# Kernel optimization log

Measured on AMD Instinct MI355X. Metric: run time of the kernel, lower is better.

## Reference

```python
import jax, jax.numpy as jnp
import numpy as np

B, Hd, Wd, C, NH, WS = 8, 128, 128, 192, 6, 8
HDIM = int(C * 2.0)   # FFN hidden = 384
RED = C // 8          # AIM channel-gate reduction = 24


def setup_inputs() -> dict:
    key = jax.random.key(0)
    ks = jax.random.split(key, 12)
    s = 0.02
    return {
        "x": jax.random.normal(ks[0], (B, Hd * Wd, C), jnp.float32),
        "H": Hd,
        "W": Wd,
        "n1_w": jnp.ones((C,), jnp.float32),
        "n1_b": jnp.zeros((C,), jnp.float32),
        "qkv_w": jax.random.normal(ks[1], (C, 3 * C), jnp.float32) * s,
        "proj_w": jax.random.normal(ks[2], (C, C), jnp.float32) * s,
        "proj_b": jnp.zeros((C,), jnp.float32),
        "attn_bias": jax.random.normal(ks[3], (NH, WS * WS, WS * WS), jnp.float32) * s,
        "conv_w": jax.random.normal(ks[4], (C, 1, 3, 3), jnp.float32) * s,
        "cg_w1": jax.random.normal(ks[5], (RED, C), jnp.float32) * s,
        "cg_w2": jax.random.normal(ks[6], (C, RED), jnp.float32) * s,
        "n2_w": jnp.ones((C,), jnp.float32),
        "n2_b": jnp.zeros((C,), jnp.float32),
        "fc1_w": jax.random.normal(ks[7], (C, HDIM), jnp.float32) * s,
        "smix_w": jax.random.normal(ks[8], (HDIM, 1, 3, 3), jnp.float32) * s,
        "fc2_w": jax.random.normal(ks[9], (HDIM, C), jnp.float32) * s,
    }


def _ln(x, w, b):
    m = x.mean(-1, keepdims=True)
    v = ((x - m) ** 2).mean(-1, keepdims=True)
    return (x - m) * jax.lax.rsqrt(v + 1e-5) * w + b


def _dwconv(x, w, H, W):
    # x: [B, L, Cx] -> depthwise 3x3 'same' conv -> [B, L, Cx]
    Bx, L, Cx = x.shape
    xi = x.transpose(0, 2, 1).reshape(Bx, Cx, H, W)
    y = jax.lax.conv_general_dilated(
        xi, w, (1, 1), 'SAME', feature_group_count=Cx,
        dimension_numbers=('NCHW', 'OIHW', 'NCHW'))
    return y.reshape(Bx, Cx, L).transpose(0, 2, 1)


def _window_attn(x, H, W, qkv_w, proj_w, proj_b, bias):
    Bx, L, Cx = x.shape
    nHw, nWw = H // WS, W // WS  # H, W are multiples of WS here (no padding needed)
    hd = Cx // NH
    # [B, L, C] -> [B*nH*nW, ws*ws, C]
    xw = (x.reshape(Bx, nHw, WS, nWw, WS, Cx)
           .transpose(0, 1, 3, 2, 4, 5)
           .reshape(Bx * nHw * nWw, WS * WS, Cx))
    qkv = (xw @ qkv_w).reshape(-1, WS * WS, 3, NH, hd).transpose(2, 0, 3, 1, 4)
    q, k, v = qkv[0], qkv[1], qkv[2]          # [Bw, nh, N, hd]
    logits = (q * hd ** -0.5) @ k.transpose(0, 1, 3, 2) + bias[None]
    attn = jax.nn.softmax(logits, axis=-1)
    out = (attn @ v).transpose(0, 2, 1, 3).reshape(-1, WS * WS, Cx)
    out = out @ proj_w + proj_b
    # windows -> [B, L, C]
    return (out.reshape(Bx, nHw, nWw, WS, WS, Cx)
               .transpose(0, 1, 3, 2, 4, 5)
               .reshape(Bx, L, Cx))


def reference(x, H, W, n1_w, n1_b, qkv_w, proj_w, proj_b, attn_bias,
              conv_w, cg_w1, cg_w2, n2_w, n2_b, fc1_w, smix_w, fc2_w):
    n1 = _ln(x, n1_w, n1_b)
    attn_feat = _window_attn(n1, H, W, qkv_w, proj_w, proj_b, attn_bias)
    conv_feat = jax.nn.gelu(_dwconv(n1, conv_w, H, W), approximate=False)
    # AIM: channel_modulates_spatial (btype == 'spatial')
    pooled = conv_feat.mean(axis=1)                                   # [B, C]
    cm = jax.nn.sigmoid(jax.nn.gelu(pooled @ cg_w1.T, approximate=False) @ cg_w2.T)
    x = x + attn_feat * cm[:, None, :] + conv_feat                    # residual (DropPath=id)
    # FFN with depthwise spatial mixing
    n2 = _ln(x, n2_w, n2_b)
    h = jax.nn.gelu(n2 @ fc1_w, approximate=False)                    # [B, L, HDIM]
    h = _dwconv(h, smix_w, H, W)
    return x + h @ fc2_w
```

## Files before the change

### kernel.cpp

```cpp
#include <hip/hip_runtime.h>
#include <hip/hip_bf16.h>
#include <math.h>

#define BATCH 8
#define CCH 192
#define LTOK 16384
#define BL 131072LL
#define NWIN 2048
#define NHEADS 6

typedef __hip_bfloat16 bf16;
typedef __bf16 bfr;
typedef bfr bf16x8 __attribute__((ext_vector_type(8)));
typedef float f32x4 __attribute__((ext_vector_type(4)));
typedef unsigned short u16x8 __attribute__((ext_vector_type(8)));
typedef unsigned short u16x4 __attribute__((ext_vector_type(4)));
typedef unsigned int u32x2 __attribute__((ext_vector_type(2)));

#define FX     0
#define FN1W   1
#define FN1B   2
#define FQKVW  3
#define FPROJW 4
#define FPROJB 5
#define FBIAS  6
#define FCONVW 7
#define FCG1   8
#define FCG2   9
#define FN2W   10
#define FN2B   11
#define FFC1   12
#define FSMIX  13
#define FFC2   14

struct InPtrs { const void* p[15]; int n[15]; };

__device__ __forceinline__ float ldin(const void* p, long long i, int f32) {
    return f32 ? ((const float*)p)[i]
               : __bfloat162float(((const bf16*)p)[i]);
}

__device__ __forceinline__ float bfcvt(unsigned short u) {
    return __uint_as_float((unsigned)u << 16);
}

__device__ __forceinline__ f32x4 ld4f(const void* p, long long i, int f32) {
    if (f32) return *(const f32x4*)((const float*)p + i);
    u16x4 v = *(const u16x4*)((const bf16*)p + i);
    f32x4 r;
    r[0] = bfcvt(v[0]); r[1] = bfcvt(v[1]); r[2] = bfcvt(v[2]); r[3] = bfcvt(v[3]);
    return r;
}
__device__ __forceinline__ f32x4 ld4b(const bf16* p, long long i) {
    u16x4 v = *(const u16x4*)(p + i);
    f32x4 r;
    r[0] = bfcvt(v[0]); r[1] = bfcvt(v[1]); r[2] = bfcvt(v[2]); r[3] = bfcvt(v[3]);
    return r;
}
__device__ __forceinline__ void st4b(bf16* p, long long i, f32x4 v) {
    union { bf16 h; unsigned short u; } cv;
    u16x4 o;
    cv.h = __float2bfloat16(v[0]); o[0] = cv.u;
    cv.h = __float2bfloat16(v[1]); o[1] = cv.u;
    cv.h = __float2bfloat16(v[2]); o[2] = cv.u;
    cv.h = __float2bfloat16(v[3]); o[3] = cv.u;
    *(u16x4*)(p + i) = o;
}

__device__ __forceinline__ unsigned pk2bf(float a, float b) {
    union { bf16 h; unsigned short u; } ca, cb;
    ca.h = __float2bfloat16(a);
    cb.h = __float2bfloat16(b);
    return (unsigned)ca.u | ((unsigned)cb.u << 16);
}

__device__ __forceinline__ float gelu_f(float v) {
    return 0.5f * v * (1.0f + erff(v * 0.70710678118654752f));
}

__device__ int local_probe(const void* p_, int n) {
    __shared__ int sh0, sh1, sh2;
    if (threadIdx.x == 0) { sh0 = 0; sh1 = 0; sh2 = 0; }
    __syncthreads();
    const bf16* p = (const bf16*)p_;
    int m = n < 2048 ? n : 2048;
    bool insane = false, evennz = false, oddnz = false;
    for (int i = threadIdx.x; i < m; i += 256) {
        float v = __bfloat162float(p[i]);
        if (!(fabsf(v) <= 1e9f)) insane = true;
        if (v != 0.0f) { if (i & 1) oddnz = true; else evennz = true; }
    }
    if (insane) sh0 = 1;
    if (evennz) sh1 = 1;
    if (oddnz)  sh2 = 1;
    __syncthreads();
    return (sh0 || (!sh1 && sh2)) ? 1 : 0;
}

__global__ __launch_bounds__(256)
void prep_k(InPtrs ip, int* __restrict__ flags,
            bf16* __restrict__ qkv_wT, bf16* __restrict__ proj_wT,
            bf16* __restrict__ fc1_wT, bf16* __restrict__ fc2_wT,
            float* __restrict__ convwT, float* __restrict__ smixwT,
            float* __restrict__ pooled) {
    int blk = blockIdx.x;
    if (blk < 15) {
        int f = local_probe(ip.p[blk], ip.n[blk]);
        if (threadIdx.x == 0) flags[blk] = f;
        return;
    }
    blk -= 15;
    if (blk < 432) {
        int f = local_probe(ip.p[FQKVW], ip.n[FQKVW]);
        int idx = blk * 256 + threadIdx.x;
        int k = idx / 576, n = idx - k * 576;
        qkv_wT[(long long)n * 192 + k] = __float2bfloat16(ldin(ip.p[FQKVW], idx, f));
        return;
    }
    blk -= 432;
    if (blk < 144) {
        int f = local_probe(ip.p[FPROJW], ip.n[FPROJW]);
        int idx = blk * 256 + threadIdx.x;
        int k = idx / 192, n = idx - k * 192;
        proj_wT[(long long)n * 192 + k] = __float2bfloat16(ldin(ip.p[FPROJW], idx, f));
        return;
    }
    blk -= 144;
    if (blk < 288) {
        int f = local_probe(ip.p[FFC1], ip.n[FFC1]);
        int idx = blk * 256 + threadIdx.x;
        int k = idx / 384, n = idx - k * 384;
        fc1_wT[(long long)n * 192 + k] = __float2bfloat16(ldin(ip.p[FFC1], idx, f));
        return;
    }
    blk -= 288;
    if (blk < 288) {
        int f = local_probe(ip.p[FFC2], ip.n[FFC2]);
        int idx = blk * 256 + threadIdx.x;
        int k = idx / 192, n = idx - k * 192;
        fc2_wT[(long long)n * 384 + k] = __float2bfloat16(ldin(ip.p[FFC2], idx, f));
        return;
    }
    blk -= 288;
    if (blk < 7) {
        int f = local_probe(ip.p[FCONVW], ip.n[FCONVW]);
        int idx = blk * 256 + threadIdx.x;
        if (idx < 192 * 9) {
            int c = idx / 9, t = idx - c * 9;
            convwT[t * 192 + c] = ldin(ip.p[FCONVW], idx, f);
        }
        return;
    }
    blk -= 7;
    if (blk < 14) {
        int f = local_probe(ip.p[FSMIX], ip.n[FSMIX]);
        int idx = blk * 256 + threadIdx.x;
        if (idx < 384 * 9) {
            int c = idx / 9, t = idx - c * 9;
            smixwT[t * 384 + c] = ldin(ip.p[FSMIX], idx, f);
        }
        return;
    }
    blk -= 14;
    {
        int idx = blk * 256 + threadIdx.x;
        if (idx < BATCH * CCH) pooled[idx] = 0.f;
    }
}

__global__ __launch_bounds__(256)
void ln_kernel(const void* __restrict__ x, const void* __restrict__ w,
               const void* __restrict__ b, bf16* __restrict__ out,
               const int* flags) {
    int fx = flags[FX], fw = flags[FN1W], fb = flags[FN1B];
    int wv = threadIdx.x >> 6, lane = threadIdx.x & 63;
    int gw = lane >> 4, l16 = lane & 15;
    long long t = (long long)blockIdx.x * 16 + wv * 4 + gw;
    long long base = t * CCH;
    f32x4 v[3];
#pragma unroll
    for (int k = 0; k < 3; ++k)
        v[k] = ld4f(x, base + l16 * 4 + 64 * k, fx);
    float s = 0.f;
#pragma unroll
    for (int k = 0; k < 3; ++k) s += v[k][0] + v[k][1] + v[k][2] + v[k][3];
    s += __shfl_xor(s, 1); s += __shfl_xor(s, 2);
    s += __shfl_xor(s, 4); s += __shfl_xor(s, 8);
    float mean = s * (1.0f / 192.0f);
    float vs = 0.f;
#pragma unroll
    for (int k = 0; k < 3; ++k)
#pragma unroll
        for (int j = 0; j < 4; ++j) {
            float d = v[k][j] - mean;
            vs += d * d;
        }
    vs += __shfl_xor(vs, 1); vs += __shfl_xor(vs, 2);
    vs += __shfl_xor(vs, 4); vs += __shfl_xor(vs, 8);
    float rstd = rsqrtf(vs * (1.0f / 192.0f) + 1e-5f);
#pragma unroll
    for (int k = 0; k < 3; ++k) {
        int c0 = l16 * 4 + 64 * k;
        f32x4 wv4 = ld4f(w, c0, fw);
        f32x4 bv4 = ld4f(b, c0, fb);
        f32x4 o;
#pragma unroll
        for (int j = 0; j < 4; ++j)
            o[j] = (v[k][j] - mean) * rstd * wv4[j] + bv4[j];
        st4b(out, base + c0, o);
    }
}

template<int EPI, int KK, int NN, typename CT>
__global__ __launch_bounds__(256)
void gemm2_k(const bf16* __restrict__ A_, const bf16* __restrict__ BT_,
             CT* __restrict__ Cmat, const void* __restrict__ bias,
             const float* __restrict__ res, const int* __restrict__ flags) {
    constexpr int KT = KK / 192;
    constexpr int NC = NN / 64;
    constexpr int NITER = NC * KT;
    constexpr int GSTR = KK * 2;
    constexpr bool WINM = (EPI == 0);
    __shared__ __align__(16) char Ts[64 * 384];

    const int fb = (EPI == 1) ? flags[FPROJB] : 0;
    const int tid = threadIdx.x;
    const int lane = tid & 63, wv = tid >> 6;
    const int r16 = lane & 15, q = lane >> 4;
    const long long m0 = (long long)blockIdx.x * 64;
    const int swz = (r16 & 7) << 4;

    const int wdx = blockIdx.x;
    const int wb = wdx >> 8, wrem = wdx & 255, wy = wrem >> 4, wx = wrem & 15;
    const long long tokbase = (long long)wb * LTOK + (wy * 8) * 128 + wx * 8;

    f32x4 pre[6];
    auto loadB = [&](int itn) {
        int nc2 = itn / KT, kt2 = itn - nc2 * KT;
#pragma unroll
        for (int p = 0; p < 6; ++p) {
            int off = p * 4096 + tid * 16;
            int row = off / 384, col = off - row * 384;
            pre[p] = *(const f32x4*)((const char*)BT_ +
                     (long long)(nc2 * 64 + row) * GSTR + kt2 * 384 + col);
        }
    };
    auto writeT = [&]() {
#pragma unroll
        for (int p = 0; p < 6; ++p) {
            int off = p * 4096 + tid * 16;
            int row = off / 384, col = off - row * 384;
            *(f32x4*)(Ts + row * 384 + (col ^ ((row & 7) << 4))) = pre[p];
        }
    };

    loadB(0);

    bf16x8 afrag[KK / 32];
    const char* Arow = Ts + (wv * 16 + r16) * 384;
    const char* asrc = (const char*)A_;
#pragma unroll
    for (int kt = 0; kt < KT; ++kt) {
#pragma unroll
        for (int p = 0; p < 6; ++p) {
            int off = p * 4096 + tid * 16;
            int row = off / 384, col = off - row * 384;
            long long grow = WINM ? (tokbase + (row >> 3) * 128 + (row & 7))
                                  : (m0 + row);
            *(f32x4*)(Ts + row * 384 + (col ^ ((row & 7) << 4))) =
                *(const f32x4*)(asrc + grow * GSTR + kt * 384 + col);
        }
        __syncthreads();
#pragma unroll
        for (int ks = 0; ks < 6; ++ks)
            afrag[kt * 6 + ks] = *(const bf16x8*)(Arow + ((ks * 64 + q * 16) ^ swz));
        __syncthreads();
    }
    writeT();
    __syncthreads();

    f32x4 acc0, acc1, acc2, acc3;
    float resv[16];

    for (int it = 0; it < NITER; ++it) {
        const int nc = it / KT, kt = it - nc * KT;
        if (kt == 0) {
            acc0 = f32x4{0.f, 0.f, 0.f, 0.f};
            acc1 = acc0; acc2 = acc0; acc3 = acc0;
            if (EPI == 3) {
#pragma unroll
                for (int j = 0; j < 4; ++j)
#pragma unroll
                    for (int r = 0; r < 4; ++r)
                        resv[j * 4 + r] =
                            res[(m0 + wv * 16 + q * 4 + r) * NN + nc * 64 + j * 16 + r16];
            }
        }
        const bool nxt = (it + 1 < NITER);
        if (nxt) loadB(it + 1);
#pragma unroll
        for (int ks = 0; ks < 6; ++ks) {
            bf16x8 a = afrag[kt * 6 + ks];
            const char* bb = Ts + r16 * 384 + ((ks * 64 + q * 16) ^ swz);
            bf16x8 b0 = *(const bf16x8*)(bb);
            bf16x8 b1 = *(const bf16x8*)(bb + 16 * 384);
            bf16x8 b2 = *(const bf16x8*)(bb + 32 * 384);
            bf16x8 b3 = *(const bf16x8*)(bb + 48 * 384);
            acc0 = __builtin_amdgcn_mfma_f32_16x16x32_bf16(a, b0, acc0, 0, 0, 0);
            acc1 = __builtin_amdgcn_mfma_f32_16x16x32_bf16(a, b1, acc1, 0, 0, 0);
            acc2 = __builtin_amdgcn_mfma_f32_16x16x32_bf16(a, b2, acc2, 0, 0, 0);
            acc3 = __builtin_amdgcn_mfma_f32_16x16x32_bf16(a, b3, acc3, 0, 0, 0);
        }
        __syncthreads();
        if (nxt) writeT();
        if (kt == KT - 1) {
            f32x4 accs[4] = {acc0, acc1, acc2, acc3};
#pragma unroll
            for (int j = 0; j < 4; ++j) {
                int col = nc * 64 + j * 16 + r16;
#pragma unroll
                for (int r = 0; r < 4; ++r) {
                    float v = accs[j][r];
                    if (EPI == 1) v += ldin(bias, col, fb);
                    if (EPI == 2) v = gelu_f(v);
                    if (EPI == 3) v += resv[j * 4 + r];
                    if (WINM) {
                        int tin = wv * 16 + q * 4 + r;
                        int sel = col / 192, rem2 = col - sel * 192;
                        int hh = rem2 >> 5, d = rem2 & 31;
                        Cmat[((((long long)sel * NWIN + wdx) * 6 + hh) * 64 + tin) * 32 + d] = (CT)v;
                    } else {
                        long long row = m0 + wv * 16 + q * 4 + r;
                        Cmat[row * NN + col] = (CT)v;
                    }
                }
            }
        }
        if (nxt) __syncthreads();
    }
}

__global__ __launch_bounds__(768)
void attn_proj_k(const bf16* __restrict__ qkvw, const void* __restrict__ bias,
                 const bf16* __restrict__ pwT, const void* __restrict__ proj_b,
                 bf16* __restrict__ attnf, const int* __restrict__ flags) {
    __shared__ __align__(16) char SM[24576];

    const int fbias = flags[FBIAS];
    const int wid = threadIdx.x >> 6, lane = threadIdx.x & 63;
    const int h = wid >> 1, half = wid & 1;
    const int w = blockIdx.x;
    const int l15 = lane & 15, quad = lane >> 4;
    bfr* vtp = (bfr*)(SM + h * 4096);

    const bfr* qb = (const bfr*)qkvw + ((long long)w * 6 + h) * 2048;
    const bfr* kb = qb + (long long)NWIN * 6 * 2048;
    const bfr* vb = kb + (long long)NWIN * 6 * 2048;

    if (half == 0) {
        const bfr* vp = vb + lane * 32;
        bf16x8 v0 = *(const bf16x8*)(vp);
        bf16x8 v1 = *(const bf16x8*)(vp + 8);
        bf16x8 v2 = *(const bf16x8*)(vp + 16);
        bf16x8 v3 = *(const bf16x8*)(vp + 24);
#pragma unroll
        for (int j = 0; j < 8; ++j) {
            int sc = lane ^ (j << 3);
            vtp[j * 64 + sc]        = v0[j];
            vtp[(j + 8) * 64 + sc]  = v1[j];
            vtp[(j + 16) * 64 + sc] = v2[j];
            vtp[(j + 24) * 64 + sc] = v3[j];
        }
    }

    bf16x8 bk[4], aq[2];
#pragma unroll
    for (int ti = 0; ti < 4; ++ti)
        bk[ti] = *(const bf16x8*)(kb + (ti * 16 + l15) * 32 + quad * 8);
#pragma unroll
    for (int tj2 = 0; tj2 < 2; ++tj2)
        aq[tj2] = *(const bf16x8*)(qb + ((half * 2 + tj2) * 16 + l15) * 32 + quad * 8);

    const float scale = 0.17677669529663689f;
    const long long bias0 = (long long)h * 4096;
    unsigned Wreg[2][4][2];
#pragma unroll
    for (int tj2 = 0; tj2 < 2; ++tj2) {
        const int tj = half * 2 + tj2;
        f32x4 T[4];
#pragma unroll
        for (int ti = 0; ti < 4; ++ti) {
            f32x4 z = {0.f, 0.f, 0.f, 0.f};
            T[ti] = __builtin_amdgcn_mfma_f32_16x16x32_bf16(bk[ti], aq[tj2], z, 0, 0, 0);
        }
        const long long brow = bias0 + (tj * 16 + l15) * 64 + quad * 4;
        float mloc = -3.0e38f;
#pragma unroll
        for (int ti = 0; ti < 4; ++ti) {
            f32x4 bv4 = ld4f(bias, brow + ti * 16, fbias);
#pragma unroll
            for (int r = 0; r < 4; ++r) {
                float v = T[ti][r] * scale + bv4[r];
                T[ti][r] = v;
                mloc = fmaxf(mloc, v);
            }
        }
        mloc = fmaxf(mloc, __shfl_xor(mloc, 16));
        mloc = fmaxf(mloc, __shfl_xor(mloc, 32));
        float l = 0.f;
#pragma unroll
        for (int ti = 0; ti < 4; ++ti)
#pragma unroll
            for (int r = 0; r < 4; ++r) {
                float e = __expf(T[ti][r] - mloc);
                T[ti][r] = e;
                l += e;
            }
        l += __shfl_xor(l, 16);
        l += __shfl_xor(l, 32);
        float linv = 1.0f / l;
#pragma unroll
        for (int ti = 0; ti < 4; ++ti) {
            Wreg[tj2][ti][0] = pk2bf(T[ti][0] * linv, T[ti][1] * linv);
            Wreg[tj2][ti][1] = pk2bf(T[ti][2] * linv, T[ti][3] * linv);
        }
    }

    __syncthreads();

    const int vsw = (l15 & 7) << 3;
    bf16x8 bv[2][2];
#pragma unroll
    for (int kc = 0; kc < 2; ++kc) {
        bv[kc][0] = *(const bf16x8*)&vtp[l15 * 64 + ((kc * 32 + quad * 8) ^ vsw)];
        bv[kc][1] = *(const bf16x8*)&vtp[(16 + l15) * 64 + ((kc * 32 + quad * 8) ^ vsw)];
    }
    const int hi = quad >> 1, qlow = quad & 1;
    f32x4 O[2][2];
#pragma unroll
    for (int tj2 = 0; tj2 < 2; ++tj2) {
        O[tj2][0] = f32x4{0.f, 0.f, 0.f, 0.f};
        O[tj2][1] = O[tj2][0];
    }
#pragma unroll
    for (int tj2 = 0; tj2 < 2; ++tj2)
#pragma unroll
        for (int kc = 0; kc < 2; ++kc) {
            union { unsigned u[4]; bf16x8 v; } ap;
#pragma unroll
            for (int j2 = 0; j2 < 4; ++j2) {
                int srcl = (2 * qlow + (j2 >> 1)) * 16 + l15;
                unsigned va = (unsigned)__shfl((int)Wreg[tj2][2 * kc][j2 & 1], srcl);
                unsigned vb2 = (unsigned)__shfl((int)Wreg[tj2][2 * kc + 1][j2 & 1], srcl);
                ap.u[j2] = hi ? vb2 : va;
            }
            O[tj2][0] = __builtin_amdgcn_mfma_f32_16x16x32_bf16(ap.v, bv[kc][0], O[tj2][0], 0, 0, 0);
            O[tj2][1] = __builtin_amdgcn_mfma_f32_16x16x32_bf16(ap.v, bv[kc][1], O[tj2][1], 0, 0, 0);
        }

    const int fpb = flags[FPROJB];
    const int pcol = wid * 16 + l15;
    float pbv = ldin(proj_b, pcol, fpb);
    bf16x8 pw[6];
#pragma unroll
    for (int ks = 0; ks < 6; ++ks)
        pw[ks] = *(const bf16x8*)((const bfr*)pwT + (long long)pcol * 192 + ks * 32 + quad * 8);

    __syncthreads();

#pragma unroll
    for (int tj2 = 0; tj2 < 2; ++tj2)
#pragma unroll
        for (int n2 = 0; n2 < 2; ++n2)
#pragma unroll
            for (int r = 0; r < 4; ++r) {
                int row = (half * 2 + tj2) * 16 + quad * 4 + r;
                int cb = (h * 64 + n2 * 32 + l15 * 2) ^ ((row & 7) << 4);
                *(bf16*)(SM + row * 384 + cb) = __float2bfloat16(O[tj2][n2][r]);
            }

    __syncthreads();

    const int csw = (l15 & 7) << 4;
    f32x4 pacc[4];
#pragma unroll
    for (int mt = 0; mt < 4; ++mt)
        pacc[mt] = f32x4{0.f, 0.f, 0.f, 0.f};
#pragma unroll
    for (int ks = 0; ks < 6; ++ks) {
#pragma unroll
        for (int mt = 0; mt < 4; ++mt) {
            bf16x8 af = *(const bf16x8*)(SM + (mt * 16 + l15) * 384 +
                                         ((ks * 64 + quad * 16) ^ csw));
            pacc[mt] = __builtin_amdgcn_mfma_f32_16x16x32_bf16(af, pw[ks], pacc[mt], 0, 0, 0);
        }
    }

#pragma unroll
    for (int mt = 0; mt < 4; ++mt)
#pragma unroll
        for (int r = 0; r < 4; ++r) {
            long long row = (long long)w * 64 + mt * 16 + quad * 4 + r;
            attnf[row * CCH + pcol] = __float2bfloat16(pacc[mt][r] + pbv);
        }
}

template<bool GELU, int CX>
__global__ __launch_bounds__(256)
void dwconv_s4_k(const bf16* __restrict__ in, const float* __restrict__ wt,
                 bf16* __restrict__ out) {
    constexpr int CG = CX / 8;
    int cpx = gridDim.x >> 3;
    int lb = (blockIdx.x & 7) * cpx + (blockIdx.x >> 3);
    long long idx = (long long)lb * 256 + threadIdx.x;
    if (idx >= (BL / 4) * CG) return;
    int cg = (int)(idx % CG);
    long long s = idx / CG;
    int xs = (int)(s & 31);
    long long by = s >> 5;
    int y = (int)(by & 127);
    int x0 = xs * 4;
    int c0 = cg * 8;
    const long long rowpix = by * 128;

    float acc[4][8] = {};
#pragma unroll
    for (int dy = -1; dy <= 1; ++dy) {
        int yy = y + dy;
        if (yy < 0 || yy > 127) continue;
        const bf16* rp = in + ((rowpix + dy * 128) + x0) * CX + c0;
        float fcol[6][8];
#pragma unroll
        for (int ci = 0; ci < 6; ++ci) {
            int xx = x0 + ci - 1;
            if (xx < 0 || xx > 127) {
#pragma unroll
                for (int j = 0; j < 8; ++j) fcol[ci][j] = 0.f;
            } else {
                u16x8 v = *(const u16x8*)(rp + (ci - 1) * CX);
#pragma unroll
                for (int j = 0; j < 8; ++j) fcol[ci][j] = bfcvt(v[j]);
            }
        }
        const float* wb = wt + (dy + 1) * 3 * CX + c0;
#pragma unroll
        for (int dx = 0; dx < 3; ++dx) {
            f32x4 w0 = *(const f32x4*)(wb + dx * CX);
            f32x4 w1 = *(const f32x4*)(wb + dx * CX + 4);
#pragma unroll
            for (int px = 0; px < 4; ++px) {
#pragma unroll
                for (int j = 0; j < 4; ++j) {
                    acc[px][j]     += fcol[px + dx][j]     * w0[j];
                    acc[px][j + 4] += fcol[px + dx][j + 4] * w1[j];
                }
            }
        }
    }
#pragma unroll
    for (int px = 0; px < 4; ++px) {
        __attribute__((aligned(16))) unsigned short ob[8];
#pragma unroll
        for (int j = 0; j < 8; ++j) {
            float vv = acc[px][j];
            if (GELU) vv = gelu_f(vv);
            union { bf16 h; unsigned short u; } cv;
            cv.h = __float2bfloat16(vv);
            ob[j] = cv.u;
        }
        *(u16x8*)(out + (rowpix + x0 + px) * CX + c0) = *(const u16x8*)ob;
    }
}

__global__ __launch_bounds__(192)
void pool_k(const bf16* __restrict__ conv, float* __restrict__ pooled) {
    __shared__ float red[8][192];
    int b = blockIdx.x, chunk = blockIdx.y;
    int cg = threadIdx.x % 24, rr = threadIdx.x / 24;
    float acc[8] = {0.f, 0.f, 0.f, 0.f, 0.f, 0.f, 0.f, 0.f};
    long long rowbase = (long long)b * LTOK + chunk * 256;
    for (int r = rr; r < 256; r += 8) {
        u16x8 v = *(const u16x8*)(conv + (rowbase + r) * CCH + cg * 8);
#pragma unroll
        for (int j = 0; j < 8; ++j) acc[j] += bfcvt(v[j]);
    }
#pragma unroll
    for (int j = 0; j < 8; ++j) red[rr][cg * 8 + j] = acc[j];
    __syncthreads();
    if (rr == 0) {
#pragma unroll
        for (int j = 0; j < 8; ++j) {
            float s = 0.f;
#pragma unroll
            for (int i = 0; i < 8; ++i) s += red[i][cg * 8 + j];
            atomicAdd(&pooled[b * CCH + cg * 8 + j], s);
        }
    }
}

__global__ void cm_k(const float* __restrict__ pooled, const void* __restrict__ w1,
                     const void* __restrict__ w2, float* __restrict__ cm,
                     const int* flags) {
    __shared__ float ps[192], g[24];
    int f1 = flags[FCG1], f2 = flags[FCG2];
    int b = blockIdx.x, c = threadIdx.x;
    ps[c] = pooled[b * CCH + c] * (1.0f / 16384.0f);
    __syncthreads();
    if (c < 24) {
        float t = 0.f;
        for (int k = 0; k < 192; ++k) t += ps[k] * ldin(w1, c * 192 + k, f1);
        g[c] = gelu_f(t);
    }
    __syncthreads();
    float s = 0.f;
#pragma unroll
    for (int r = 0; r < 24; ++r) s += g[r] * ldin(w2, c * 24 + r, f2);
    cm[b * CCH + c] = 1.0f / (1.0f + expf(-s));
}

__global__ __launch_bounds__(256)
void x2ln2_k(const void* __restrict__ x, const bf16* __restrict__ attnf,
             const bf16* __restrict__ conv, const float* __restrict__ cm,
             const void* __restrict__ w, const void* __restrict__ bb,
             float* __restrict__ x2, bf16* __restrict__ n2, const int* flags) {
    int fx = flags[FX], fw = flags[FN2W], fb = flags[FN2B];
    int wv = threadIdx.x >> 6, lane = threadIdx.x & 63;
    int gw = lane >> 4, l16 = lane & 15;
    long long t = (long long)blockIdx.x * 16 + wv * 4 + gw;
    int b = (int)(t >> 14);
    int l = (int)(t & 16383);
    int y = l >> 7, xx = l & 127;
    long long wrow = ((long long)b * 256 + (y >> 3) * 16 + (xx >> 3)) * 64 + (y & 7) * 8 + (xx & 7);

    f32x4 sv[3];
#pragma unroll
    for (int k = 0; k < 3; ++k) {
        int c0 = l16 * 4 + 64 * k;
        f32x4 xv  = ld4f(x, t * CCH + c0, fx);
        f32x4 af  = ld4b(attnf, wrow * CCH + c0);
        f32x4 cf  = ld4b(conv, t * CCH + c0);
        f32x4 cmv = *(const f32x4*)(cm + b * CCH + c0);
        f32x4 o;
#pragma unroll
        for (int j = 0; j < 4; ++j)
            o[j] = xv[j] + af[j] * cmv[j] + cf[j];
        *(f32x4*)(x2 + t * CCH + c0) = o;
        sv[k] = o;
    }
    float s = 0.f;
#pragma unroll
    for (int k = 0; k < 3; ++k) s += sv[k][0] + sv[k][1] + sv[k][2] + sv[k][3];
    s += __shfl_xor(s, 1); s += __shfl_xor(s, 2);
    s += __shfl_xor(s, 4); s += __shfl_xor(s, 8);
    float mean = s * (1.0f / 192.0f);
    float vs = 0.f;
#pragma unroll
    for (int k = 0; k < 3; ++k)
#pragma unroll
        for (int j = 0; j < 4; ++j) {
            float d = sv[k][j] - mean;
            vs += d * d;
        }
    vs += __shfl_xor(vs, 1); vs += __shfl_xor(vs, 2);
    vs += __shfl_xor(vs, 4); vs += __shfl_xor(vs, 8);
    float rstd = rsqrtf(vs * (1.0f / 192.0f) + 1e-5f);
#pragma unroll
    for (int k = 0; k < 3; ++k) {
        int c0 = l16 * 4 + 64 * k;
        f32x4 wv4 = ld4f(w, c0, fw);
        f32x4 bv4 = ld4f(bb, c0, fb);
        f32x4 o;
#pragma unroll
        for (int j = 0; j < 4; ++j)
            o[j] = (sv[k][j] - mean) * rstd * wv4[j] + bv4[j];
        st4b(n2, t * CCH + c0, o);
    }
}

extern "C" void kernel_launch(void* const* d_in, const int* in_sizes, int n_in,
                              void* d_out, int out_size, void* d_ws, size_t ws_size,
                              hipStream_t stream) {
    (void)n_in; (void)out_size; (void)ws_size;
    float* out = (float*)d_out;

    char* wsp = (char*)d_ws;
    size_t off = 0;
    auto alloc = [&](size_t bytes) -> char* {
        char* p = wsp + off;
        off += (bytes + 255) & ~(size_t)255;
        return p;
    };
    int*  flags   = (int*)alloc(15 * 4);
    bf16* qkv_wT  = (bf16*)alloc(576 * 192 * 2);
    bf16* proj_wT = (bf16*)alloc(192 * 192 * 2);
    bf16* fc1_wT  = (bf16*)alloc(384 * 192 * 2);
    bf16* fc2_wT  = (bf16*)alloc(192 * 384 * 2);
    float* convwT = (float*)alloc(9 * CCH * 4);
    float* smixwT = (float*)alloc(9 * 384 * 4);
    float* pooled = (float*)alloc(BATCH * CCH * 4);
    float* cm     = (float*)alloc(BATCH * CCH * 4);
    char* Rbig    = alloc(BL * 576 * 2);
    char* Rpair   = alloc(BL * 384 * 2);

    bf16* qkvb  = (bf16*)Rbig;
    bf16* convf = (bf16*)Rbig;
    bf16* hbuf  = (bf16*)Rbig;
    bf16* n1    = (bf16*)Rpair;
    bf16* attnf = (bf16*)(Rpair + (size_t)BL * 192 * 2);
    bf16* n2    = n1;
    bf16* h2    = (bf16*)Rpair;
    float* x2   = out;

    const int imap[15] = {0, 3, 4, 5, 6, 7, 8, 9, 10, 11, 12, 13, 14, 15, 16};
    InPtrs ip;
    for (int i = 0; i < 15; ++i) { ip.p[i] = d_in[imap[i]]; ip.n[i] = in_sizes[imap[i]]; }
    const void* x        = d_in[0];
    const void* proj_b   = d_in[7];
    const void* attnbias = d_in[8];
    const void* cg_w1    = d_in[10];
    const void* cg_w2    = d_in[11];

    prep_k<<<1194, 256, 0, stream>>>(ip, flags, qkv_wT, proj_wT, fc1_wT, fc2_wT,
                                     convwT, smixwT, pooled);

    ln_kernel<<<BL / 16, 256, 0, stream>>>(x, d_in[3], d_in[4], n1, flags);
    gemm2_k<0, 192, 576, bf16><<<BL / 64, 256, 0, stream>>>(n1, qkv_wT, qkvb, nullptr, nullptr, flags);
    attn_proj_k<<<NWIN, 768, 0, stream>>>(qkvb, attnbias, proj_wT, proj_b, attnf, flags);
    dwconv_s4_k<true, 192><<<(int)(BL / 4 * 24 / 256), 256, 0, stream>>>(n1, convwT, convf);
    pool_k<<<dim3(BATCH, 64), 192, 0, stream>>>(convf, pooled);
    cm_k<<<BATCH, 192, 0, stream>>>(pooled, cg_w1, cg_w2, cm, flags);
    x2ln2_k<<<BL / 16, 256, 0, stream>>>(x, attnf, convf, cm, d_in[12], d_in[13], x2, n2, flags);
    gemm2_k<2, 192, 384, bf16><<<BL / 64, 256, 0, stream>>>(n2, fc1_wT, hbuf, nullptr, nullptr, flags);
    dwconv_s4_k<false, 384><<<(int)(BL / 4 * 48 / 256), 256, 0, stream>>>(hbuf, smixwT, h2);
    gemm2_k<3, 384, 192, float><<<BL / 64, 256, 0, stream>>>(h2, fc2_wT, out, nullptr, x2, flags);
}
```

Before: 591.3 us.

## Fuse channel pooling into dwconv and gate MLP into x2/LN2 kernel

The global average pool of the GELU conv output is now accumulated inside the depthwise conv kernel through shared-memory atomics and one global atomic per channel per block. The separate pool kernel is removed. The small channel-gate MLP (cm_k) is recomputed redundantly at the start of every x2ln2 block from the pooled sums. This removes two launches and a full re-read of the conv feature map, but adds an extra sync plus a 192x24 dot loop to each of the many x2ln2 blocks. The pool now sums fp32 values before bf16 rounding, and the idx bounds check was dropped.

Result: slower. 707.0 us (+19.6%).

```diff
diff --git a/kernel.cpp b/kernel.cpp
--- a/kernel.cpp
+++ b/kernel.cpp
@@ -505,15 +505,19 @@
         }
 }
 
-template<bool GELU, int CX>
+template<bool GELU, int CX, bool POOL>
 __global__ __launch_bounds__(256)
 void dwconv_s4_k(const bf16* __restrict__ in, const float* __restrict__ wt,
-                 bf16* __restrict__ out) {
+                 bf16* __restrict__ out, float* __restrict__ pooled) {
     constexpr int CG = CX / 8;
+    __shared__ float psum[POOL ? 192 : 1];
+    if (POOL) {
+        if (threadIdx.x < 192) psum[threadIdx.x] = 0.f;
+        __syncthreads();
+    }
     int cpx = gridDim.x >> 3;
     int lb = (blockIdx.x & 7) * cpx + (blockIdx.x >> 3);
     long long idx = (long long)lb * 256 + threadIdx.x;
-    if (idx >= (BL / 4) * CG) return;
     int cg = (int)(idx % CG);
     long long s = idx / CG;
     int xs = (int)(s & 31);
@@ -557,6 +561,7 @@
             }
         }
     }
+    float sums[8] = {0.f, 0.f, 0.f, 0.f, 0.f, 0.f, 0.f, 0.f};
 #pragma unroll
     for (int px = 0; px < 4; ++px) {
         __attribute__((aligned(16))) unsigned short ob[8];
@@ -564,66 +569,53 @@
         for (int j = 0; j < 8; ++j) {
             float vv = acc[px][j];
             if (GELU) vv = gelu_f(vv);
+            if (POOL) sums[j] += vv;
             union { bf16 h; unsigned short u; } cv;
             cv.h = __float2bfloat16(vv);
             ob[j] = cv.u;
         }
         *(u16x8*)(out + (rowpix + x0 + px) * CX + c0) = *(const u16x8*)ob;
     }
-}
-
-__global__ __launch_bounds__(192)
-void pool_k(const bf16* __restrict__ conv, float* __restrict__ pooled) {
-    __shared__ float red[8][192];
-    int b = blockIdx.x, chunk = blockIdx.y;
-    int cg = threadIdx.x % 24, rr = threadIdx.x / 24;
-    float acc[8] = {0.f, 0.f, 0.f, 0.f, 0.f, 0.f, 0.f, 0.f};
-    long long rowbase = (long long)b * LTOK + chunk * 256;
-    for (int r = rr; r < 256; r += 8) {
-        u16x8 v = *(const u16x8*)(conv + (rowbase + r) * CCH + cg * 8);
-#pragma unroll
-        for (int j = 0; j < 8; ++j) acc[j] += bfcvt(v[j]);
-    }
-#pragma unroll
-    for (int j = 0; j < 8; ++j) red[rr][cg * 8 + j] = acc[j];
-    __syncthreads();
-    if (rr == 0) {
-#pragma unroll
-        for (int j = 0; j < 8; ++j) {
-            float s = 0.f;
-#pragma unroll
-            for (int i = 0; i < 8; ++i) s += red[i][cg * 8 + j];
-            atomicAdd(&pooled[b * CCH + cg * 8 + j], s);
-        }
-    }
-}
-
-__global__ void cm_k(const float* __restrict__ pooled, const void* __restrict__ w1,
-                     const void* __restrict__ w2, float* __restrict__ cm,
-                     const int* flags) {
-    __shared__ float ps[192], g[24];
-    int f1 = flags[FCG1], f2 = flags[FCG2];
-    int b = blockIdx.x, c = threadIdx.x;
-    ps[c] = pooled[b * CCH + c] * (1.0f / 16384.0f);
-    __syncthreads();
-    if (c < 24) {
-        float t = 0.f;
-        for (int k = 0; k < 192; ++k) t += ps[k] * ldin(w1, c * 192 + k, f1);
-        g[c] = gelu_f(t);
-    }
-    __syncthreads();
-    float s = 0.f;
-#pragma unroll
-    for (int r = 0; r < 24; ++r) s += g[r] * ldin(w2, c * 24 + r, f2);
-    cm[b * CCH + c] = 1.0f / (1.0f + expf(-s));
+    if (POOL) {
+#pragma unroll
+        for (int j = 0; j < 8; ++j)
+            atomicAdd(&psum[c0 + j], sums[j]);
+        __syncthreads();
+        if (threadIdx.x < 192) {
+            int b = (int)(by >> 7);
+            atomicAdd(&pooled[b * CCH + threadIdx.x], psum[threadIdx.x]);
+        }
+    }
 }
 
 __global__ __launch_bounds__(256)
 void x2ln2_k(const void* __restrict__ x, const bf16* __restrict__ attnf,
-             const bf16* __restrict__ conv, const float* __restrict__ cm,
+             const bf16* __restrict__ conv, const float* __restrict__ pooled,
+             const void* __restrict__ w1, const void* __restrict__ w2,
              const void* __restrict__ w, const void* __restrict__ bb,
              float* __restrict__ x2, bf16* __restrict__ n2, const int* flags) {
+    __shared__ float ps[192], g[24], cms[192];
     int fx = flags[FX], fw = flags[FN2W], fb = flags[FN2B];
+    int f1 = flags[FCG1], f2 = flags[FCG2];
+    const int b0 = (int)(((long long)blockIdx.x * 16) >> 14);
+
+    int tid = threadIdx.x;
+    if (tid < 192) ps[tid] = pooled[b0 * CCH + tid] * (1.0f / 16384.0f);
+    __syncthreads();
+    if (tid < 24) {
+        float t = 0.f;
+        for (int k = 0; k < 192; ++k) t += ps[k] * ldin(w1, tid * 192 + k, f1);
+        g[tid] = gelu_f(t);
+    }
+    __syncthreads();
+    if (tid < 192) {
+        float s2 = 0.f;
+#pragma unroll
+        for (int r = 0; r < 24; ++r) s2 += g[r] * ldin(w2, tid * 24 + r, f2);
+        cms[tid] = 1.0f / (1.0f + expf(-s2));
+    }
+    __syncthreads();
+
     int wv = threadIdx.x >> 6, lane = threadIdx.x & 63;
     int gw = lane >> 4, l16 = lane & 15;
     long long t = (long long)blockIdx.x * 16 + wv * 4 + gw;
@@ -639,7 +631,7 @@
         f32x4 xv  = ld4f(x, t * CCH + c0, fx);
         f32x4 af  = ld4b(attnf, wrow * CCH + c0);
         f32x4 cf  = ld4b(conv, t * CCH + c0);
-        f32x4 cmv = *(const f32x4*)(cm + b * CCH + c0);
+        f32x4 cmv = *(const f32x4*)(cms + c0);
         f32x4 o;
 #pragma unroll
         for (int j = 0; j < 4; ++j)
@@ -698,7 +690,6 @@
     float* convwT = (float*)alloc(9 * CCH * 4);
     float* smixwT = (float*)alloc(9 * 384 * 4);
     float* pooled = (float*)alloc(BATCH * CCH * 4);
-    float* cm     = (float*)alloc(BATCH * CCH * 4);
     char* Rbig    = alloc(BL * 576 * 2);
     char* Rpair   = alloc(BL * 384 * 2);
 
@@ -726,11 +717,10 @@
     ln_kernel<<<BL / 16, 256, 0, stream>>>(x, d_in[3], d_in[4], n1, flags);
     gemm2_k<0, 192, 576, bf16><<<BL / 64, 256, 0, stream>>>(n1, qkv_wT, qkvb, nullptr, nullptr, flags);
     attn_proj_k<<<NWIN, 768, 0, stream>>>(qkvb, attnbias, proj_wT, proj_b, attnf, flags);
-    dwconv_s4_k<true, 192><<<(int)(BL / 4 * 24 / 256), 256, 0, stream>>>(n1, convwT, convf);
-    pool_k<<<dim3(BATCH, 64), 192, 0, stream>>>(convf, pooled);
-    cm_k<<<BATCH, 192, 0, stream>>>(pooled, cg_w1, cg_w2, cm, flags);
-    x2ln2_k<<<BL / 16, 256, 0, stream>>>(x, attnf, convf, cm, d_in[12], d_in[13], x2, n2, flags);
+    dwconv_s4_k<true, 192, true><<<(int)(BL / 4 * 24 / 256), 256, 0, stream>>>(n1, convwT, convf, pooled);
+    x2ln2_k<<<BL / 16, 256, 0, stream>>>(x, attnf, convf, pooled, cg_w1, cg_w2,
+                                         d_in[12], d_in[13], x2, n2, flags);
     gemm2_k<2, 192, 384, bf16><<<BL / 64, 256, 0, stream>>>(n2, fc1_wT, hbuf, nullptr, nullptr, flags);
-    dwconv_s4_k<false, 384><<<(int)(BL / 4 * 48 / 256), 256, 0, stream>>>(hbuf, smixwT, h2);
+    dwconv_s4_k<false, 384, false><<<(int)(BL / 4 * 48 / 256), 256, 0, stream>>>(hbuf, smixwT, h2, nullptr);
     gemm2_k<3, 384, 192, float><<<BL / 64, 256, 0, stream>>>(h2, fc2_wT, out, nullptr, x2, flags);
 }
```
